# Optimization experiments

Measured on AMD Instinct MI355X. Metric: run time of the kernel, lower is better.

The kernel has to match this reference:

```python
import jax, jax.numpy as jnp
import numpy as np

N_NODES = 10000
N_EDGES = 160000
F_IN, D, DEPTH, F_OUT = 6, 512, 10, 1


def setup_inputs() -> dict:
    key = jax.random.key(0)
    ks = jax.random.split(key, 10)
    features = jax.random.normal(ks[0], (N_NODES, F_IN), dtype=jnp.float32)
    src = jax.random.randint(ks[1], (N_EDGES,), 0, N_NODES, dtype=jnp.int32)
    dst = jax.random.randint(ks[2], (N_EDGES,), 0, N_NODES, dtype=jnp.int32)
    s_in = 1.0 / np.sqrt(F_IN)
    s_h = 1.0 / np.sqrt(D)
    W_in = jax.random.uniform(ks[3], (F_IN, D), jnp.float32, -s_in, s_in)
    b_in = jax.random.uniform(ks[4], (D,), jnp.float32, -s_in, s_in)
    Ws = jax.random.uniform(ks[5], (DEPTH, D, D), jnp.float32, -s_h, s_h)
    bs = jax.random.uniform(ks[6], (DEPTH, D), jnp.float32, -s_h, s_h)
    W_out = jax.random.uniform(ks[7], (D, F_OUT), jnp.float32, -s_h, s_h)
    b_out = jax.random.uniform(ks[8], (F_OUT,), jnp.float32, -s_h, s_h)
    return {"features": features, "W_in": W_in, "b_in": b_in, "Ws": Ws,
            "bs": bs, "W_out": W_out, "b_out": b_out, "src": src, "dst": dst}


def reference(features, W_in, b_in, Ws, bs, W_out, b_out, src, dst):
    n = features.shape[0]
    # GCNLayer: aggregate = scatter-sum of neighbor features (copy_src + sum), then Linear
    agg = jax.ops.segment_sum(features[src], dst, num_segments=n)  # [N, F_in]
    x = jax.nn.relu(agg @ W_in + b_in)  # ReLU only after input layer (per forward)

    def step(x, wb):
        W, b = wb
        a = jax.ops.segment_sum(x[src], dst, num_segments=n)  # [N, D]
        return a @ W + b, None  # no activation between hidden GCN layers

    x, _ = jax.lax.scan(step, x, (Ws, bs))
    return x @ W_out + b_out  # [N, 1]
```

## Files before the change

kernel.cpp:

```cpp
#include <hip/hip_runtime.h>

#define N_NODES 10000
#define N_EDGES 160000
#define DVAL    512
#define DEPTH   10



__global__ void zero_int_kernel(int* p, int n) {
    int i = blockIdx.x * 256 + threadIdx.x;
    if (i < n) p[i] = 0;
}

__global__ void count_deg_kernel(const int* __restrict__ dst, int* __restrict__ deg, int n) {
    int i = blockIdx.x * 256 + threadIdx.x;
    if (i < n) atomicAdd(&deg[dst[i]], 1);
}

__global__ __launch_bounds__(1024) void scan_kernel(const int* __restrict__ deg,
                                                    int* __restrict__ row_ptr,
                                                    int* __restrict__ cursor) {
    __shared__ int sums[1024];
    const int tid = threadIdx.x;
    const int CH = 10;
    int base = tid * CH;
    int local[CH];
    int s = 0;
#pragma unroll
    for (int i = 0; i < CH; i++) {
        int idx = base + i;
        int v = (idx < N_NODES) ? deg[idx] : 0;
        local[i] = s;
        s += v;
    }
    sums[tid] = s;
    __syncthreads();
    for (int off = 1; off < 1024; off <<= 1) {
        int v = (tid >= off) ? sums[tid - off] : 0;
        __syncthreads();
        sums[tid] += v;
        __syncthreads();
    }
    int chunk_base = (tid > 0) ? sums[tid - 1] : 0;
#pragma unroll
    for (int i = 0; i < CH; i++) {
        int idx = base + i;
        if (idx < N_NODES) {
            int v = chunk_base + local[i];
            row_ptr[idx] = v;
            cursor[idx] = v;
        }
    }
    if (tid == 1023) row_ptr[N_NODES] = sums[1023];
}

__global__ void fill_edges_kernel(const int* __restrict__ src, const int* __restrict__ dst,
                                  int* __restrict__ cursor, int* __restrict__ esrc, int n) {
    int i = blockIdx.x * 256 + threadIdx.x;
    if (i < n) {
        int p = atomicAdd(&cursor[dst[i]], 1);
        esrc[p] = src[i];
    }
}

__global__ __launch_bounds__(256) void matvec_gamma_kernel(const float* __restrict__ W,
                                                           const float* __restrict__ b,
                                                           const float* __restrict__ v_in,
                                                           float* __restrict__ v_out,
                                                           float* __restrict__ gamma_slot) {
    const int gw = (blockIdx.x * 256 + threadIdx.x) >> 6;
    const int lane = threadIdx.x & 63;
    {
        const float* row = W + (size_t)gw * 512;
        float s = 0.f;
#pragma unroll
        for (int c = 0; c < 8; c++) s += row[lane + c * 64] * v_in[lane + c * 64];
#pragma unroll
        for (int off = 32; off > 0; off >>= 1) s += __shfl_down(s, off, 64);
        if (lane == 0) v_out[gw] = s;
    }
    if (gw == 511) {
        float s = 0.f;
#pragma unroll
        for (int c = 0; c < 8; c++) s += b[lane + c * 64] * v_in[lane + c * 64];
#pragma unroll
        for (int off = 32; off > 0; off >>= 1) s += __shfl_down(s, off, 64);
        if (lane == 0) *gamma_slot = s;
    }
}

__global__ __launch_bounds__(256) void aggregate6_kernel(const float* __restrict__ feat,
                                                         const int* __restrict__ row_ptr,
                                                         const int* __restrict__ esrc,
                                                         float* __restrict__ agg6) {
    int t = blockIdx.x * 256 + threadIdx.x;
    int node = t >> 3;
    int c = t & 7;
    if (node >= N_NODES || c >= 6) return;
    int start = row_ptr[node], end = row_ptr[node + 1];
    float a0 = 0.f, a1 = 0.f;
    int e = start;
    for (; e + 2 <= end; e += 2) {
        a0 += feat[esrc[e] * 6 + c];
        a1 += feat[esrc[e + 1] * 6 + c];
    }
    if (e < end) a0 += feat[esrc[e] * 6 + c];
    agg6[node * 6 + c] = a0 + a1;
}

__global__ __launch_bounds__(256) void input_z_kernel(const float* __restrict__ agg6,
                                                      const float* __restrict__ W_in,
                                                      const float* __restrict__ b_in,
                                                      const float* __restrict__ vtilde,
                                                      float* __restrict__ z) {
    __shared__ float red[4];
    const int node = blockIdx.x;
    const int j = threadIdx.x;
    const int lane = j & 63;
    const int wave = j >> 6;
    float a[6];
#pragma unroll
    for (int k = 0; k < 6; k++) a[k] = agg6[node * 6 + k];
    float s = 0.f;
#pragma unroll
    for (int r = 0; r < 2; r++) {
        int jj = j + r * 256;
        float t = b_in[jj];
#pragma unroll
        for (int k = 0; k < 6; k++) t += a[k] * W_in[k * 512 + jj];
        s += fmaxf(t, 0.f) * vtilde[jj];
    }
#pragma unroll
    for (int off = 32; off > 0; off >>= 1) s += __shfl_down(s, off, 64);
    if (lane == 0) red[wave] = s;
    __syncthreads();
    if (j == 0) z[node] = (red[0] + red[1]) + (red[2] + red[3]);
}

__global__ __launch_bounds__(256) void col_agg_kernel(const float* __restrict__ r_in,
                                                      const int* __restrict__ row_ptr,
                                                      const int* __restrict__ esrc,
                                                      const float* __restrict__ gamma,
                                                      int gi,
                                                      const float* __restrict__ b_out,
                                                      int is_last,
                                                      float* __restrict__ r_out) {
    int i = blockIdx.x * 256 + threadIdx.x;
    if (i >= N_NODES) return;
    int s = row_ptr[i], e = row_ptr[i + 1];
    float a0 = 0.f, a1 = 0.f, a2 = 0.f, a3 = 0.f;
    int p = s;
    for (; p + 4 <= e; p += 4) {
        int i0 = esrc[p], i1 = esrc[p + 1], i2 = esrc[p + 2], i3 = esrc[p + 3];
        a0 += r_in[i0];
        a1 += r_in[i1];
        a2 += r_in[i2];
        a3 += r_in[i3];
    }
    for (; p < e; p++) a0 += r_in[esrc[p]];
    float res = (a0 + a1) + (a2 + a3) + gamma[gi];
    if (is_last) res += b_out[0];
    r_out[i] = res;
}


extern "C" void kernel_launch(void* const* d_in, const int* in_sizes, int n_in,
                              void* d_out, int out_size, void* d_ws, size_t ws_size,
                              hipStream_t stream) {
    const float* features = (const float*)d_in[0];
    const float* W_in     = (const float*)d_in[1];
    const float* b_in     = (const float*)d_in[2];
    const float* Ws       = (const float*)d_in[3];
    const float* bs       = (const float*)d_in[4];
    const float* W_out    = (const float*)d_in[5];
    const float* b_out    = (const float*)d_in[6];
    const int*   src      = (const int*)d_in[7];
    const int*   dst      = (const int*)d_in[8];
    float* out = (float*)d_out;

    char* p = (char*)d_ws;
    auto alloc = [&](size_t bytes) {
        char* r = p;
        p += (bytes + 255) & ~size_t(255);
        return r;
    };
    int* deg     = (int*)alloc((size_t)N_NODES * 4);
    int* row_ptr = (int*)alloc((size_t)(N_NODES + 1) * 4);
    int* cursor  = (int*)alloc((size_t)N_NODES * 4);
    int* esrc    = (int*)alloc((size_t)N_EDGES * 4);
    float* agg6  = (float*)alloc((size_t)N_NODES * 6 * 4);
    float* v_a   = (float*)alloc(512 * 4);
    float* v_b   = (float*)alloc(512 * 4);
    float* gamma = (float*)alloc(DEPTH * 4);
    float* r_a   = (float*)alloc((size_t)N_NODES * 4);
    float* r_b   = (float*)alloc((size_t)N_NODES * 4);

    zero_int_kernel<<<(N_NODES + 255) / 256, 256, 0, stream>>>(deg, N_NODES);
    count_deg_kernel<<<(N_EDGES + 255) / 256, 256, 0, stream>>>(dst, deg, N_EDGES);
    scan_kernel<<<1, 1024, 0, stream>>>(deg, row_ptr, cursor);
    fill_edges_kernel<<<(N_EDGES + 255) / 256, 256, 0, stream>>>(src, dst, cursor, esrc, N_EDGES);

    hipMemcpyAsync(v_a, W_out, 512 * sizeof(float), hipMemcpyDeviceToDevice, stream);
    float* v_cur = v_a;
    float* v_nxt = v_b;
    for (int l = DEPTH - 1; l >= 0; l--) {
        matvec_gamma_kernel<<<128, 256, 0, stream>>>(Ws + (size_t)l * 512 * 512,
                                                     bs + (size_t)l * 512,
                                                     v_cur, v_nxt, gamma + l);
        float* t = v_cur; v_cur = v_nxt; v_nxt = t;
    }

    aggregate6_kernel<<<(N_NODES * 8 + 255) / 256, 256, 0, stream>>>(features, row_ptr, esrc, agg6);
    input_z_kernel<<<N_NODES, 256, 0, stream>>>(agg6, W_in, b_in, v_cur, r_a);

    float* r_cur = r_a;
    float* r_nxt = r_b;
    for (int l = 0; l < DEPTH; l++) {
        int last = (l == DEPTH - 1);
        col_agg_kernel<<<(N_NODES + 255) / 256, 256, 0, stream>>>(
            r_cur, row_ptr, esrc, gamma, l, b_out, last, last ? out : r_nxt);
        float* t = r_cur; r_cur = r_nxt; r_nxt = t;
    }
}
```

Measured before the change: 195.6 us.

## Fuse all stages into one persistent kernel with grid barriers and concurrent groups

```diff
diff --git a/kernel.cpp b/kernel.cpp
--- a/kernel.cpp
+++ b/kernel.cpp
@@ -2,165 +2,195 @@
 
 #define N_NODES 10000
 #define N_EDGES 160000
-#define DVAL    512
 #define DEPTH   10
-
-
-
-__global__ void zero_int_kernel(int* p, int n) {
-    int i = blockIdx.x * 256 + threadIdx.x;
-    if (i < n) p[i] = 0;
-}
-
-__global__ void count_deg_kernel(const int* __restrict__ dst, int* __restrict__ deg, int n) {
-    int i = blockIdx.x * 256 + threadIdx.x;
-    if (i < n) atomicAdd(&deg[dst[i]], 1);
-}
-
-__global__ __launch_bounds__(1024) void scan_kernel(const int* __restrict__ deg,
-                                                    int* __restrict__ row_ptr,
-                                                    int* __restrict__ cursor) {
-    __shared__ int sums[1024];
+#define NBLK    256
+#define NTHR    512
+#define GRPA    64
+#define GRPB    (NBLK - GRPA)
+#define RPAD    10048
+
+#define CA 0
+#define CB 12
+#define CF 16
+
+
+__global__ void zero_ctr_kernel(int* c) {
+    if (threadIdx.x < 32) c[threadIdx.x] = 0;
+}
+
+__device__ inline void gbar(int* c, int expected) {
+    __syncthreads();
+    if (threadIdx.x == 0) {
+        __threadfence();
+        __hip_atomic_fetch_add(c, 1, __ATOMIC_ACQ_REL, __HIP_MEMORY_SCOPE_AGENT);
+        while (__hip_atomic_load(c, __ATOMIC_ACQUIRE, __HIP_MEMORY_SCOPE_AGENT) < expected)
+            __builtin_amdgcn_s_sleep(8);
+        __threadfence();
+    }
+    __syncthreads();
+}
+
+__device__ inline float wave_reduce(float s) {
+#pragma unroll
+    for (int off = 32; off > 0; off >>= 1) s += __shfl_down(s, off, 64);
+    return s;
+}
+
+__global__ __launch_bounds__(NTHR) void mega_kernel(
+    const float* __restrict__ features, const float* __restrict__ W_in,
+    const float* __restrict__ b_in, const float* __restrict__ Ws,
+    const float* __restrict__ bs, const float* __restrict__ W_out,
+    const float* __restrict__ b_out, const int* __restrict__ src,
+    const int* __restrict__ dst, float* __restrict__ out,
+    int* __restrict__ ctr, int* __restrict__ deg, int* __restrict__ row_ptr,
+    int* __restrict__ cursor, int* __restrict__ esrc, float* __restrict__ agg6,
+    float* __restrict__ v,
+    float* __restrict__ gamma,
+    float* __restrict__ r) {
+    __shared__ int sums[NTHR];
+    const int blk = blockIdx.x;
     const int tid = threadIdx.x;
-    const int CH = 10;
-    int base = tid * CH;
-    int local[CH];
-    int s = 0;
-#pragma unroll
-    for (int i = 0; i < CH; i++) {
-        int idx = base + i;
-        int v = (idx < N_NODES) ? deg[idx] : 0;
-        local[i] = s;
-        s += v;
-    }
-    sums[tid] = s;
-    __syncthreads();
-    for (int off = 1; off < 1024; off <<= 1) {
-        int v = (tid >= off) ? sums[tid - off] : 0;
-        __syncthreads();
-        sums[tid] += v;
-        __syncthreads();
-    }
-    int chunk_base = (tid > 0) ? sums[tid - 1] : 0;
-#pragma unroll
-    for (int i = 0; i < CH; i++) {
-        int idx = base + i;
-        if (idx < N_NODES) {
-            int v = chunk_base + local[i];
-            row_ptr[idx] = v;
-            cursor[idx] = v;
-        }
-    }
-    if (tid == 1023) row_ptr[N_NODES] = sums[1023];
-}
-
-__global__ void fill_edges_kernel(const int* __restrict__ src, const int* __restrict__ dst,
-                                  int* __restrict__ cursor, int* __restrict__ esrc, int n) {
-    int i = blockIdx.x * 256 + threadIdx.x;
-    if (i < n) {
-        int p = atomicAdd(&cursor[dst[i]], 1);
-        esrc[p] = src[i];
-    }
-}
-
-__global__ __launch_bounds__(256) void matvec_gamma_kernel(const float* __restrict__ W,
-                                                           const float* __restrict__ b,
-                                                           const float* __restrict__ v_in,
-                                                           float* __restrict__ v_out,
-                                                           float* __restrict__ gamma_slot) {
-    const int gw = (blockIdx.x * 256 + threadIdx.x) >> 6;
-    const int lane = threadIdx.x & 63;
+
+    if (blk < GRPA) {
+        const int g = blk * NTHR + tid;
+        const int w = g >> 6;
+        const int lane = g & 63;
+        if (g < 512) v[g] = W_out[g];
+        gbar(ctr + CA + 0, GRPA);
+        int cur = 0;
+        for (int l = DEPTH - 1; l >= 0; l--) {
+            const float* Wrow = Ws + (size_t)l * 512 * 512 + (size_t)w * 512;
+            const float* vin = v + cur * 512;
+            float s = 0.f;
+#pragma unroll
+            for (int c = 0; c < 8; c++) s += Wrow[lane + c * 64] * vin[lane + c * 64];
+            s = wave_reduce(s);
+            if (lane == 0) v[(cur ^ 1) * 512 + w] = s;
+            if (w == 511) {
+                const float* bl = bs + (size_t)l * 512;
+                float t = 0.f;
+#pragma unroll
+                for (int c = 0; c < 8; c++) t += bl[lane + c * 64] * vin[lane + c * 64];
+                t = wave_reduce(t);
+                if (lane == 0) gamma[l] = t;
+            }
+            gbar(ctr + CA + 1 + (DEPTH - 1 - l), GRPA);
+            cur ^= 1;
+        }
+    } else {
+        const int g = (blk - GRPA) * NTHR + tid;
+        if (g < N_NODES) deg[g] = 0;
+        gbar(ctr + CB + 0, GRPB);
+        for (int i = g; i < N_EDGES; i += GRPB * NTHR) atomicAdd(&deg[dst[i]], 1);
+        gbar(ctr + CB + 1, GRPB);
+        if (blk == GRPA) {
+            const int CH = 20;
+            int base = tid * CH;
+            int local[CH];
+            int s = 0;
+#pragma unroll
+            for (int i = 0; i < CH; i++) {
+                int idx = base + i;
+                int vv = (idx < N_NODES) ? deg[idx] : 0;
+                local[i] = s;
+                s += vv;
+            }
+            sums[tid] = s;
+            __syncthreads();
+            for (int off = 1; off < NTHR; off <<= 1) {
+                int vv = (tid >= off) ? sums[tid - off] : 0;
+                __syncthreads();
+                sums[tid] += vv;
+                __syncthreads();
+            }
+            int cb = (tid > 0) ? sums[tid - 1] : 0;
+#pragma unroll
+            for (int i = 0; i < CH; i++) {
+                int idx = base + i;
+                if (idx < N_NODES) {
+                    int vv = cb + local[i];
+                    row_ptr[idx] = vv;
+                    cursor[idx] = vv;
+                }
+            }
+            if (tid == NTHR - 1) row_ptr[N_NODES] = sums[NTHR - 1];
+        }
+        gbar(ctr + CB + 2, GRPB);
+        for (int i = g; i < N_EDGES; i += GRPB * NTHR) {
+            int p = atomicAdd(&cursor[dst[i]], 1);
+            esrc[p] = src[i];
+        }
+        gbar(ctr + CB + 3, GRPB);
+        {
+            int node = g >> 3, c = g & 7;
+            if (node < N_NODES && c < 6) {
+                int s0 = row_ptr[node], e0 = row_ptr[node + 1];
+                float a0 = 0.f, a1 = 0.f;
+                int e = s0;
+                for (; e + 2 <= e0; e += 2) {
+                    a0 += features[esrc[e] * 6 + c];
+                    a1 += features[esrc[e + 1] * 6 + c];
+                }
+                if (e < e0) a0 += features[esrc[e] * 6 + c];
+                agg6[node * 6 + c] = a0 + a1;
+            }
+        }
+    }
+
+    gbar(ctr + CF + 0, NBLK);
+
     {
-        const float* row = W + (size_t)gw * 512;
-        float s = 0.f;
-#pragma unroll
-        for (int c = 0; c < 8; c++) s += row[lane + c * 64] * v_in[lane + c * 64];
-#pragma unroll
-        for (int off = 32; off > 0; off >>= 1) s += __shfl_down(s, off, 64);
-        if (lane == 0) v_out[gw] = s;
-    }
-    if (gw == 511) {
-        float s = 0.f;
-#pragma unroll
-        for (int c = 0; c < 8; c++) s += b[lane + c * 64] * v_in[lane + c * 64];
-#pragma unroll
-        for (int off = 32; off > 0; off >>= 1) s += __shfl_down(s, off, 64);
-        if (lane == 0) *gamma_slot = s;
-    }
-}
-
-__global__ __launch_bounds__(256) void aggregate6_kernel(const float* __restrict__ feat,
-                                                         const int* __restrict__ row_ptr,
-                                                         const int* __restrict__ esrc,
-                                                         float* __restrict__ agg6) {
-    int t = blockIdx.x * 256 + threadIdx.x;
-    int node = t >> 3;
-    int c = t & 7;
-    if (node >= N_NODES || c >= 6) return;
-    int start = row_ptr[node], end = row_ptr[node + 1];
-    float a0 = 0.f, a1 = 0.f;
-    int e = start;
-    for (; e + 2 <= end; e += 2) {
-        a0 += feat[esrc[e] * 6 + c];
-        a1 += feat[esrc[e + 1] * 6 + c];
-    }
-    if (e < end) a0 += feat[esrc[e] * 6 + c];
-    agg6[node * 6 + c] = a0 + a1;
-}
-
-__global__ __launch_bounds__(256) void input_z_kernel(const float* __restrict__ agg6,
-                                                      const float* __restrict__ W_in,
-                                                      const float* __restrict__ b_in,
-                                                      const float* __restrict__ vtilde,
-                                                      float* __restrict__ z) {
-    __shared__ float red[4];
-    const int node = blockIdx.x;
-    const int j = threadIdx.x;
-    const int lane = j & 63;
-    const int wave = j >> 6;
-    float a[6];
-#pragma unroll
-    for (int k = 0; k < 6; k++) a[k] = agg6[node * 6 + k];
-    float s = 0.f;
-#pragma unroll
-    for (int r = 0; r < 2; r++) {
-        int jj = j + r * 256;
-        float t = b_in[jj];
-#pragma unroll
-        for (int k = 0; k < 6; k++) t += a[k] * W_in[k * 512 + jj];
-        s += fmaxf(t, 0.f) * vtilde[jj];
-    }
-#pragma unroll
-    for (int off = 32; off > 0; off >>= 1) s += __shfl_down(s, off, 64);
-    if (lane == 0) red[wave] = s;
-    __syncthreads();
-    if (j == 0) z[node] = (red[0] + red[1]) + (red[2] + red[3]);
-}
-
-__global__ __launch_bounds__(256) void col_agg_kernel(const float* __restrict__ r_in,
-                                                      const int* __restrict__ row_ptr,
-                                                      const int* __restrict__ esrc,
-                                                      const float* __restrict__ gamma,
-                                                      int gi,
-                                                      const float* __restrict__ b_out,
-                                                      int is_last,
-                                                      float* __restrict__ r_out) {
-    int i = blockIdx.x * 256 + threadIdx.x;
-    if (i >= N_NODES) return;
-    int s = row_ptr[i], e = row_ptr[i + 1];
-    float a0 = 0.f, a1 = 0.f, a2 = 0.f, a3 = 0.f;
-    int p = s;
-    for (; p + 4 <= e; p += 4) {
-        int i0 = esrc[p], i1 = esrc[p + 1], i2 = esrc[p + 2], i3 = esrc[p + 3];
-        a0 += r_in[i0];
-        a1 += r_in[i1];
-        a2 += r_in[i2];
-        a3 += r_in[i3];
-    }
-    for (; p < e; p++) a0 += r_in[esrc[p]];
-    float res = (a0 + a1) + (a2 + a3) + gamma[gi];
-    if (is_last) res += b_out[0];
-    r_out[i] = res;
+        const int g = blk * NTHR + tid;
+        const int wgid = g >> 6;
+        const int lane = g & 63;
+        const int nw = (NBLK * NTHR) >> 6;
+        for (int node = wgid; node < N_NODES; node += nw) {
+            float a[6];
+#pragma unroll
+            for (int k = 0; k < 6; k++) a[k] = agg6[node * 6 + k];
+            float s = 0.f;
+#pragma unroll
+            for (int c8 = 0; c8 < 8; c8++) {
+                int j = lane + c8 * 64;
+                float t = b_in[j];
+#pragma unroll
+                for (int k = 0; k < 6; k++) t += a[k] * W_in[k * 512 + j];
+                s += fmaxf(t, 0.f) * v[j];
+            }
+            s = wave_reduce(s);
+            if (lane == 0) r[node] = s;
+        }
+    }
+    gbar(ctr + CF + 1, NBLK);
+
+    {
+        const int g = blk * NTHR + tid;
+        const int node = g >> 3;
+        const int l8 = g & 7;
+        int start = 0, end = 0;
+        if (node < N_NODES) {
+            start = row_ptr[node];
+            end = row_ptr[node + 1];
+        }
+        int cur = 0;
+        for (int l = 0; l < DEPTH; l++) {
+            const float* rin = r + cur * RPAD;
+            float s = 0.f;
+            if (node < N_NODES) {
+                for (int e = start + l8; e < end; e += 8) s += rin[esrc[e]];
+            }
+            s += __shfl_xor(s, 1, 64);
+            s += __shfl_xor(s, 2, 64);
+            s += __shfl_xor(s, 4, 64);
+            if (node < N_NODES && l8 == 0) {
+                float res = s + gamma[l];
+                if (l == DEPTH - 1) out[node] = res + b_out[0];
+                else r[(cur ^ 1) * RPAD + node] = res;
+            }
+            if (l < DEPTH - 1) gbar(ctr + CF + 2 + l, NBLK);
+            cur ^= 1;
+        }
+    }
 }
 
 
@@ -184,41 +214,19 @@
         p += (bytes + 255) & ~size_t(255);
         return r;
     };
+    int* ctr     = (int*)alloc(32 * 4);
     int* deg     = (int*)alloc((size_t)N_NODES * 4);
     int* row_ptr = (int*)alloc((size_t)(N_NODES + 1) * 4);
     int* cursor  = (int*)alloc((size_t)N_NODES * 4);
     int* esrc    = (int*)alloc((size_t)N_EDGES * 4);
     float* agg6  = (float*)alloc((size_t)N_NODES * 6 * 4);
-    float* v_a   = (float*)alloc(512 * 4);
-    float* v_b   = (float*)alloc(512 * 4);
+    float* v     = (float*)alloc(2 * 512 * 4);
     float* gamma = (float*)alloc(DEPTH * 4);
-    float* r_a   = (float*)alloc((size_t)N_NODES * 4);
-    float* r_b   = (float*)alloc((size_t)N_NODES * 4);
-
-    zero_int_kernel<<<(N_NODES + 255) / 256, 256, 0, stream>>>(deg, N_NODES);
-    count_deg_kernel<<<(N_EDGES + 255) / 256, 256, 0, stream>>>(dst, deg, N_EDGES);
-    scan_kernel<<<1, 1024, 0, stream>>>(deg, row_ptr, cursor);
-    fill_edges_kernel<<<(N_EDGES + 255) / 256, 256, 0, stream>>>(src, dst, cursor, esrc, N_EDGES);
-
-    hipMemcpyAsync(v_a, W_out, 512 * sizeof(float), hipMemcpyDeviceToDevice, stream);
-    float* v_cur = v_a;
-    float* v_nxt = v_b;
-    for (int l = DEPTH - 1; l >= 0; l--) {
-        matvec_gamma_kernel<<<128, 256, 0, stream>>>(Ws + (size_t)l * 512 * 512,
-                                                     bs + (size_t)l * 512,
-                                                     v_cur, v_nxt, gamma + l);
-        float* t = v_cur; v_cur = v_nxt; v_nxt = t;
-    }
-
-    aggregate6_kernel<<<(N_NODES * 8 + 255) / 256, 256, 0, stream>>>(features, row_ptr, esrc, agg6);
-    input_z_kernel<<<N_NODES, 256, 0, stream>>>(agg6, W_in, b_in, v_cur, r_a);
-
-    float* r_cur = r_a;
-    float* r_nxt = r_b;
-    for (int l = 0; l < DEPTH; l++) {
-        int last = (l == DEPTH - 1);
-        col_agg_kernel<<<(N_NODES + 255) / 256, 256, 0, stream>>>(
-            r_cur, row_ptr, esrc, gamma, l, b_out, last, last ? out : r_nxt);
-        float* t = r_cur; r_cur = r_nxt; r_nxt = t;
-    }
-}
+    float* r     = (float*)alloc((size_t)2 * RPAD * 4);
+
+    zero_ctr_kernel<<<1, 64, 0, stream>>>(ctr);
+    mega_kernel<<<NBLK, NTHR, 0, stream>>>(features, W_in, b_in, Ws, bs, W_out,
+                                           b_out, src, dst, out, ctr, deg,
+                                           row_ptr, cursor, esrc, agg6, v,
+                                           gamma, r);
+}
```

New measurement: 705.5 us. +260.7%, slower.
